# Performance work log

Measured on AMD Instinct MI355X. Metric: run time of the kernel, lower is better.

The kernel has to match this reference:

```python
import jax, jax.numpy as jnp
import numpy as np

EOS_IDX = 2
B, LAYERS, HEADS, SEQ = 1, 33, 20, 512


def setup_inputs() -> dict:
    key = jax.random.key(0)
    k1, k2, k3, k4 = jax.random.split(key, 4)
    tokens = jax.random.randint(k1, (B, SEQ), 0, 30)
    attentions = jax.random.normal(k2, (B, LAYERS, HEADS, SEQ, SEQ), dtype=jnp.float32)
    weight = jax.random.normal(k3, (LAYERS * HEADS,), dtype=jnp.float32) * 0.05
    bias = jax.random.normal(k4, (1,), dtype=jnp.float32) * 0.05
    return {"tokens": tokens, "attentions": attentions, "weight": weight, "bias": bias}


def reference(tokens, attentions, weight, bias):
    b, nl, nh, s, _ = attentions.shape
    # mask out positions at/after EOS token pairs
    eos = (tokens != EOS_IDX).astype(attentions.dtype)           # [B, S]
    mask2d = eos[:, None, :] * eos[:, :, None]                   # [B, S, S]
    att = attentions * mask2d[:, None, None, :, :]
    # [..., :-1, :-1] then [..., 1:, 1:] == drop first and last positions
    att = att[..., 1:-1, 1:-1]                                   # [B, L, H, S-2, S-2]
    att = att.reshape(b, nl * nh, s - 2, s - 2)                  # [B, F, s2, s2]
    # symmetrize
    sym = att + jnp.swapaxes(att, -1, -2)
    # average product correction
    a1 = sym.sum(-1, keepdims=True)                              # [B, F, s2, 1]
    a2 = sym.sum(-2, keepdims=True)                              # [B, F, 1, s2]
    a12 = sym.sum((-1, -2), keepdims=True)                       # [B, F, 1, 1]
    norm = sym - a1 * a2 / a12
    logits = jnp.einsum('bfij,f->bij', norm, weight) + bias[0]
    return jax.nn.sigmoid(logits)                                # [B, s2, s2]
```

## Files before the change

kernel.cpp:

```cpp
#include <hip/hip_runtime.h>
#include <math.h>

#define SEQ   512
#define NF    660
#define CROP  510
#define EOSI  2
#define RT    16
#define GH    20
#define NT_   32
#define NG    33

typedef float f4 __attribute__((ext_vector_type(4)));
typedef float f2 __attribute__((ext_vector_type(2)));

#define BARRIER_LGKM() asm volatile("s_waitcnt lgkmcnt(0)\n\ts_barrier" ::: "memory")

#define LOADP(buf, f, prow) do {                                              \
    const float* _b = A + ((size_t)(f) << 18) + ((size_t)(prow) << 9);        \
    buf[0] = *(const f4*)(_b + 4 * lane);                                     \
    buf[1] = *(const f4*)(_b + 256 + 4 * lane);                               \
    buf[2] = *(const f4*)(_b + 512 + 4 * lane);                               \
    buf[3] = *(const f4*)(_b + 768 + 4 * lane);                               \
} while (0)

#define COMP(buf, wf, cacc, wa, POFF, f) do {                                 \
    _Pragma("unroll")                                                         \
    for (int rr = 0; rr < 2; ++rr) {                                          \
        const float mi = mrow[(POFF) * 2 + rr];                               \
        f4 x0 = buf[2 * rr], x1 = buf[2 * rr + 1];                            \
        float vals[8] = {x0[0], x0[1], x0[2], x0[3],                          \
                         x1[0], x1[1], x1[2], x1[3]};                         \
        float rs = 0.f;                                                       \
        _Pragma("unroll")                                                     \
        for (int e = 0; e < 8; ++e) {                                         \
            const float v = vals[e];                                          \
            wa[rr][e] += (wf) * v;                                            \
            rs += mskv[e] * v;                                                \
            cacc[e] += mi * v;                                                \
        }                                                                     \
        _Pragma("unroll")                                                     \
        for (int off = 32; off > 0; off >>= 1)                                \
            rs += __shfl_down(rs, off, 64);                                   \
        if (lane == 0)                                                        \
            rowsum[((size_t)(f) << 9) + row0 + (POFF) * 2 + rr] = rs;         \
    }                                                                         \
} while (0)

__global__ __launch_bounds__(256) void pass1_kernel(
    const float* __restrict__ A, const int* __restrict__ tokens,
    const float* __restrict__ weight,
    float* __restrict__ WApart, float* __restrict__ rowsum, float* __restrict__ colpart)
{
    __shared__ float msk[SEQ];
    __shared__ float col_lds[2][4][2][SEQ];

    const int t = blockIdx.x, g = blockIdx.y;
    const int tid = threadIdx.x, wave = tid >> 6, lane = tid & 63;

    for (int j = tid; j < SEQ; j += 256)
        msk[j] = (j >= 1 && j <= SEQ - 2 && tokens[j] != EOSI) ? 1.f : 0.f;
    BARRIER_LGKM();

    float mskv[8];
    #pragma unroll
    for (int e = 0; e < 8; ++e)
        mskv[e] = msk[(e >> 2) * 256 + 4 * lane + (e & 3)];

    const int row0 = t * RT + wave * 4;
    const float mrow[4] = {msk[row0], msk[row0 + 1], msk[row0 + 2], msk[row0 + 3]};

    float waLo[2][8], waHi[2][8];
    #pragma unroll
    for (int r = 0; r < 2; ++r)
        #pragma unroll
        for (int e = 0; e < 8; ++e) { waLo[r][e] = 0.f; waHi[r][e] = 0.f; }

    f4 bufA[4], bufB[4];
    const int fbase = g * GH;
    LOADP(bufA, fbase, row0);

    for (int hp = 0; hp < 10; ++hp) {
        const int fa = fbase + 2 * hp, fb = fa + 1;
        const float wf0 = weight[fa], wf1 = weight[fb];
        float caccA[8] = {0, 0, 0, 0, 0, 0, 0, 0};
        float caccB[8] = {0, 0, 0, 0, 0, 0, 0, 0};

        LOADP(bufB, fa, row0 + 2);
        COMP(bufA, wf0, caccA, waLo, 0, fa);
        LOADP(bufA, fb, row0);
        COMP(bufB, wf0, caccA, waHi, 1, fa);
        LOADP(bufB, fb, row0 + 2);
        COMP(bufA, wf1, caccB, waLo, 0, fb);
        if (hp < 9) LOADP(bufA, fa + 2, row0);
        COMP(bufB, wf1, caccB, waHi, 1, fb);

        const int pp = hp & 1;
        #pragma unroll
        for (int e = 0; e < 8; ++e) {
            const int c = (e >> 2) * 256 + 4 * lane + (e & 3);
            col_lds[pp][wave][0][c] = caccA[e];
            col_lds[pp][wave][1][c] = caccB[e];
        }
        BARRIER_LGKM();
        #pragma unroll
        for (int h = 0; h < 2; ++h) {
            const int c = 2 * tid;
            f2 s;
            s[0] = col_lds[pp][0][h][c]     + col_lds[pp][1][h][c]
                 + col_lds[pp][2][h][c]     + col_lds[pp][3][h][c];
            s[1] = col_lds[pp][0][h][c + 1] + col_lds[pp][1][h][c + 1]
                 + col_lds[pp][2][h][c + 1] + col_lds[pp][3][h][c + 1];
            *(f2*)(colpart + ((size_t)t * NF + fa + h) * SEQ + c) = s;
        }
    }

    float* __restrict__ wp = WApart + (size_t)g * SEQ * SEQ;
    #pragma unroll
    for (int rr = 0; rr < 2; ++rr) {
        f4 l0 = {waLo[rr][0], waLo[rr][1], waLo[rr][2], waLo[rr][3]};
        f4 l1 = {waLo[rr][4], waLo[rr][5], waLo[rr][6], waLo[rr][7]};
        *(f4*)(wp + ((size_t)(row0 + rr) << 9) + 4 * lane) = l0;
        *(f4*)(wp + ((size_t)(row0 + rr) << 9) + 256 + 4 * lane) = l1;
        f4 h0 = {waHi[rr][0], waHi[rr][1], waHi[rr][2], waHi[rr][3]};
        f4 h1 = {waHi[rr][4], waHi[rr][5], waHi[rr][6], waHi[rr][7]};
        *(f4*)(wp + ((size_t)(row0 + 2 + rr) << 9) + 4 * lane) = h0;
        *(f4*)(wp + ((size_t)(row0 + 2 + rr) << 9) + 256 + 4 * lane) = h1;
    }
}

__global__ __launch_bounds__(512) void kernel2(
    const float* __restrict__ WApart, float* __restrict__ WA,
    const float* __restrict__ rowsum, const float* __restrict__ colpart,
    const int* __restrict__ tokens, const float* __restrict__ weight,
    float* __restrict__ a1, float* __restrict__ sfac)
{
    __shared__ float part[8];
    const int b = blockIdx.x, tid = threadIdx.x;
    if (b < 128) {
        const size_t idx4 = (size_t)b * 512 + tid;
        f4 a = *(const f4*)(WApart + 4 * idx4);
        #pragma unroll 8
        for (int g = 1; g < NG; ++g) {
            f4 x = *(const f4*)(WApart + (size_t)g * (SEQ * SEQ) + 4 * idx4);
            a += x;
        }
        *(f4*)(WA + 4 * idx4) = a;
    } else {
        const int f = b - 128, j = tid;
        float cs = 0.f;
        #pragma unroll 8
        for (int t = 0; t < NT_; ++t)
            cs += colpart[((size_t)t * NF + f) * SEQ + j];
        const float m = (j >= 1 && j <= SEQ - 2 && tokens[j] != EOSI) ? 1.f : 0.f;
        const float v = m * (rowsum[((size_t)f << 9) + j] + cs);
        a1[((size_t)f << 9) + j] = v;
        float s = v;
        #pragma unroll
        for (int off = 32; off > 0; off >>= 1)
            s += __shfl_down(s, off, 64);
        const int wave = tid >> 6, lane = tid & 63;
        if (lane == 0) part[wave] = s;
        __syncthreads();
        if (tid == 0) {
            float a12 = 0.f;
            #pragma unroll
            for (int k = 0; k < 8; ++k) a12 += part[k];
            sfac[f] = weight[f] / a12;
        }
    }
}

__global__ __launch_bounds__(256) void pass3_kernel(
    const float* __restrict__ WA, const float* __restrict__ a1,
    const float* __restrict__ sfac, const int* __restrict__ tokens,
    const float* __restrict__ bias, float* __restrict__ out)
{
    const int TI = blockIdx.y * 16;
    const int TJ = blockIdx.x * 16;
    const int tid = threadIdx.x;
    const int tx = tid & 15, ty = tid >> 4;

    __shared__ float u_s[32][17];
    __shared__ float v_s[32][17];

    float acc = 0.f;

    for (int f0 = 0; f0 < NF; f0 += 32) {
        #pragma unroll
        for (int c = 0; c < 4; ++c) {
            const int e = c * 256 + tid;
            const int arr = e >> 9, ff = (e >> 4) & 31, ii = e & 15;
            const int f = f0 + ff;
            float val = 0.f;
            if (f < NF) {
                if (arr == 0) {
                    int Iu = TI + 1 + ii; if (Iu > SEQ - 1) Iu = SEQ - 1;
                    val = a1[((size_t)f << 9) + Iu] * sfac[f];
                } else {
                    int Ju = TJ + 1 + ii; if (Ju > SEQ - 1) Ju = SEQ - 1;
                    val = a1[((size_t)f << 9) + Ju];
                }
            }
            if (arr == 0) u_s[ff][ii] = val; else v_s[ff][ii] = val;
        }
        __syncthreads();
        #pragma unroll
        for (int ff = 0; ff < 32; ++ff)
            acc += u_s[ff][ty] * v_s[ff][tx];
        __syncthreads();
    }

    const int i = TI + ty, j = TJ + tx;
    if (i < CROP && j < CROP) {
        const int I = i + 1, J = j + 1;
        const float mi = (tokens[I] != EOSI) ? 1.f : 0.f;
        const float mj = (tokens[J] != EOSI) ? 1.f : 0.f;
        const float first = mi * mj * (WA[((size_t)I << 9) + J] + WA[((size_t)J << 9) + I]);
        const float logit = first - acc + bias[0];
        out[(size_t)i * CROP + j] = 1.f / (1.f + expf(-logit));
    }
}

extern "C" void kernel_launch(void* const* d_in, const int* in_sizes, int n_in,
                              void* d_out, int out_size, void* d_ws, size_t ws_size,
                              hipStream_t stream) {
    const int*   tokens = (const int*)d_in[0];
    const float* A      = (const float*)d_in[1];
    const float* weight = (const float*)d_in[2];
    const float* bias   = (const float*)d_in[3];
    float* out = (float*)d_out;

    float* WApart  = (float*)d_ws;
    float* colpart = WApart + (size_t)NG * SEQ * SEQ;
    float* WA      = colpart + (size_t)NT_ * NF * SEQ;
    float* rowsum  = WA + (size_t)SEQ * SEQ;
    float* a1      = rowsum + (size_t)NF * SEQ;
    float* sfac    = a1 + (size_t)NF * SEQ;

    dim3 g1(NT_, NG);
    pass1_kernel<<<g1, 256, 0, stream>>>(A, tokens, weight, WApart, rowsum, colpart);

    kernel2<<<128 + NF, 512, 0, stream>>>(WApart, WA, rowsum, colpart, tokens, weight, a1, sfac);

    dim3 g3(32, 32);
    pass3_kernel<<<g3, 256, 0, stream>>>(WA, a1, sfac, tokens, bias, out);
}
```

Baseline: 220.6 us.

## Stage column and row partial sums in LDS and write them out coalesced at end

The pass-1 loop now processes one feature per iteration instead of two. Column partial sums are accumulated into a 20x512 LDS staging array and row sums into a small LDS array. Both are flushed to global memory after the loop with wide coalesced stores, replacing scattered per-iteration stores and single-lane row-sum writes. The cost is about 40KB more LDS per block, which may lower occupancy, twice as many barriers, and a shallower prefetch pipeline.

```diff
diff --git a/kernel.cpp b/kernel.cpp
--- a/kernel.cpp
+++ b/kernel.cpp
@@ -23,7 +23,7 @@
     buf[3] = *(const f4*)(_b + 768 + 4 * lane);                               \
 } while (0)
 
-#define COMP(buf, wf, cacc, wa, POFF, f) do {                                 \
+#define COMP(buf, wf, cacc, wa, POFF, h) do {                                 \
     _Pragma("unroll")                                                         \
     for (int rr = 0; rr < 2; ++rr) {                                          \
         const float mi = mrow[(POFF) * 2 + rr];                               \
@@ -42,7 +42,7 @@
         for (int off = 32; off > 0; off >>= 1)                                \
             rs += __shfl_down(rs, off, 64);                                   \
         if (lane == 0)                                                        \
-            rowsum[((size_t)(f) << 9) + row0 + (POFF) * 2 + rr] = rs;         \
+            rowstage[h][wave * 4 + (POFF) * 2 + rr] = rs;                     \
     }                                                                         \
 } while (0)
 
@@ -52,7 +52,9 @@
     float* __restrict__ WApart, float* __restrict__ rowsum, float* __restrict__ colpart)
 {
     __shared__ float msk[SEQ];
-    __shared__ float col_lds[2][4][2][SEQ];
+    __shared__ float col_lds[2][4][SEQ];
+    __shared__ float colstage[GH][SEQ];
+    __shared__ float rowstage[GH][RT];
 
     const int t = blockIdx.x, g = blockIdx.y;
     const int tid = threadIdx.x, wave = tid >> 6, lane = tid & 63;
@@ -79,41 +81,51 @@
     const int fbase = g * GH;
     LOADP(bufA, fbase, row0);
 
-    for (int hp = 0; hp < 10; ++hp) {
-        const int fa = fbase + 2 * hp, fb = fa + 1;
-        const float wf0 = weight[fa], wf1 = weight[fb];
-        float caccA[8] = {0, 0, 0, 0, 0, 0, 0, 0};
-        float caccB[8] = {0, 0, 0, 0, 0, 0, 0, 0};
-
-        LOADP(bufB, fa, row0 + 2);
-        COMP(bufA, wf0, caccA, waLo, 0, fa);
-        LOADP(bufA, fb, row0);
-        COMP(bufB, wf0, caccA, waHi, 1, fa);
-        LOADP(bufB, fb, row0 + 2);
-        COMP(bufA, wf1, caccB, waLo, 0, fb);
-        if (hp < 9) LOADP(bufA, fa + 2, row0);
-        COMP(bufB, wf1, caccB, waHi, 1, fb);
-
-        const int pp = hp & 1;
-        #pragma unroll
-        for (int e = 0; e < 8; ++e) {
-            const int c = (e >> 2) * 256 + 4 * lane + (e & 3);
-            col_lds[pp][wave][0][c] = caccA[e];
-            col_lds[pp][wave][1][c] = caccB[e];
-        }
+    for (int h = 0; h < GH; ++h) {
+        const int f = fbase + h;
+        const float wf = weight[f];
+        float cacc[8] = {0, 0, 0, 0, 0, 0, 0, 0};
+
+        LOADP(bufB, f, row0 + 2);
+        COMP(bufA, wf, cacc, waLo, 0, h);
+        if (h < GH - 1) LOADP(bufA, f + 1, row0);
+        COMP(bufB, wf, cacc, waHi, 1, h);
+
+        const int pp = h & 1;
+        #pragma unroll
+        for (int e = 0; e < 8; ++e)
+            col_lds[pp][wave][(e >> 2) * 256 + 4 * lane + (e & 3)] = cacc[e];
         BARRIER_LGKM();
-        #pragma unroll
-        for (int h = 0; h < 2; ++h) {
+        {
             const int c = 2 * tid;
             f2 s;
-            s[0] = col_lds[pp][0][h][c]     + col_lds[pp][1][h][c]
-                 + col_lds[pp][2][h][c]     + col_lds[pp][3][h][c];
-            s[1] = col_lds[pp][0][h][c + 1] + col_lds[pp][1][h][c + 1]
-                 + col_lds[pp][2][h][c + 1] + col_lds[pp][3][h][c + 1];
-            *(f2*)(colpart + ((size_t)t * NF + fa + h) * SEQ + c) = s;
-        }
-    }
-
+            s[0] = col_lds[pp][0][c]     + col_lds[pp][1][c]
+                 + col_lds[pp][2][c]     + col_lds[pp][3][c];
+            s[1] = col_lds[pp][0][c + 1] + col_lds[pp][1][c + 1]
+                 + col_lds[pp][2][c + 1] + col_lds[pp][3][c + 1];
+            *(f2*)&colstage[h][c] = s;
+        }
+    }
+
+    BARRIER_LGKM();
+
+    {
+        float* __restrict__ dst = colpart + ((size_t)t * NF + fbase) * SEQ;
+        const float* __restrict__ srcl = &colstage[0][0];
+        #pragma unroll
+        for (int it = 0; it < 10; ++it) {
+            const int fl = (it * 256 + tid) * 4;
+            *(f4*)(dst + fl) = *(const f4*)(srcl + fl);
+        }
+    }
+    #pragma unroll
+    for (int it = 0; it < 2; ++it) {
+        const int e = it * 256 + tid;
+        if (e < GH * RT) {
+            const int h = e >> 4, r = e & 15;
+            rowsum[((size_t)(fbase + h) << 9) + t * RT + r] = rowstage[h][r];
+        }
+    }
     float* __restrict__ wp = WApart + (size_t)g * SEQ * SEQ;
     #pragma unroll
     for (int rr = 0; rr < 2; ++rr) {
```

Measured after the change: 215.7 us. 2.2% less time.
